# Kernel optimization log

Measured on AMD Instinct MI355X. Metric: run time of the kernel, lower is better.

The kernel has to match this reference:

```python
import jax, jax.numpy as jnp
import numpy as np
from jax import lax

B, C, L = 32, 64, 16384
C_OUT = 64


def conv1d(x, w, b):
    # x: [B,C,L], w: [Cout,Cin,K], b: [Cout]
    y = lax.conv_general_dilated(x, w, window_strides=(1,), padding='VALID',
                                 dimension_numbers=('NCH', 'OIH', 'NCH'))
    return y + b[None, :, None]


def setup_inputs() -> dict:
    key = jax.random.key(0)
    k1, k2, k3, k4, k5 = jax.random.split(key, 5)
    x = jax.random.normal(k1, (B, C, L), dtype=jnp.float32)
    # kernel_size = 1 (see shape_source); PyTorch Conv1d default init scale ~ 1/sqrt(Cin*K)
    s = 1.0 / np.sqrt(C * 1)
    offset_w = jax.random.uniform(k2, (C * 1, C, 1), jnp.float32, -s, s)
    offset_b = jax.random.uniform(k3, (C * 1,), jnp.float32, -s, s)
    regular_w = jax.random.uniform(k4, (C_OUT, C, 1), jnp.float32, -s, s)
    regular_b = jax.random.uniform(k5, (C_OUT,), jnp.float32, -s, s)
    return {'x': x, 'offset_w': offset_w, 'offset_b': offset_b,
            'regular_w': regular_w, 'regular_b': regular_b}


def reference(x, offset_w, offset_b, regular_w, regular_b):
    Bx, Cx, Lx = x.shape
    offsets = conv1d(x, offset_w, offset_b)                 # [B,C,L]
    base = jnp.arange(Lx, dtype=x.dtype)[None, None, :]      # [1,1,L]
    indices = jnp.clip(base + offsets, 0.0, Lx - 1)          # [B,C,L] float positions
    idx_floor = jnp.floor(indices)
    idx_ceil = jnp.ceil(indices)
    x_floor = jnp.take_along_axis(x, idx_floor.astype(jnp.int32), axis=2)
    x_ceil = jnp.take_along_axis(x, idx_ceil.astype(jnp.int32), axis=2)
    frac = indices - idx_floor
    x_deform = (1.0 - frac) * x_floor + frac * x_ceil        # [B,C,L]
    return conv1d(x_deform, regular_w, regular_b)            # [B,Cout,L]
```

## Files before the change

kernel.cpp:

```cpp
#include <hip/hip_runtime.h>


#define BDIM 256
#define BB   32
#define CC   64
#define LL   16384
#define TL   64
#define HH   4
#define ROWS (TL + 2*HH)
#define RSW  36
#define RSH  72

typedef __fp16 half_t;
typedef __attribute__((ext_vector_type(2))) __fp16 h2;
typedef __attribute__((ext_vector_type(8))) __fp16 h8;
typedef __attribute__((ext_vector_type(4))) float f4;

union H2U { h2 h; unsigned u; };
union H8U { unsigned u[4]; h8 v; };

static __device__ __forceinline__ unsigned pk(float a, float b) {
    H2U r; r.h = __builtin_amdgcn_cvt_pkrtz(a, b); return r.u;
}

static __device__ __forceinline__ void load_a_split(const float* __restrict__ wp,
                                                    int row, int ks, int q,
                                                    h8* ahi, h8* alo) {
    const float* base = wp + row * 64 + ks * 32 + q * 8;
    float4 w0 = *(const float4*)base;
    float4 w1 = *(const float4*)(base + 4);
    float v[8] = {w0.x, w0.y, w0.z, w0.w, w1.x, w1.y, w1.z, w1.w};
    H8U h, l;
    #pragma unroll
    for (int p = 0; p < 4; ++p) {
        H2U hh; hh.h = __builtin_amdgcn_cvt_pkrtz(v[2*p], v[2*p+1]);
        h.u[p] = hh.u;
        l.u[p] = pk(v[2*p] - (float)hh.h[0], v[2*p+1] - (float)hh.h[1]);
    }
    *ahi = h.v; *alo = l.v;
}

static __device__ __forceinline__ h8 load_a_f16(const float* __restrict__ wp,
                                                int row, int ks, int q) {
    const float* base = wp + row * 64 + ks * 32 + q * 8;
    float4 w0 = *(const float4*)base;
    float4 w1 = *(const float4*)(base + 4);
    float v[8] = {w0.x, w0.y, w0.z, w0.w, w1.x, w1.y, w1.z, w1.w};
    H8U r;
    #pragma unroll
    for (int p = 0; p < 4; ++p) r.u[p] = pk(v[2*p], v[2*p+1]);
    return r.v;
}

__global__ __launch_bounds__(BDIM)
void deform_conv1d_r5(const float* __restrict__ x,
                      const float* __restrict__ offw,
                      const float* __restrict__ offb,
                      const float* __restrict__ regw,
                      const float* __restrict__ regb,
                      float* __restrict__ out) {
    __shared__ __align__(16) unsigned char smem[10368 + 9216];
    unsigned* XtH = (unsigned*)smem;
    unsigned* XdW = (unsigned*)(smem + 10368);
    half_t*   XtHh = (half_t*)smem;
    half_t*   Xdh  = (half_t*)(smem + 10368);
    (void)Xdh;

    const int tid = threadIdx.x;
    const int bx  = blockIdx.x;
    const int lg0 = bx * TL;
    const int b   = blockIdx.y;
    const size_t xb = (size_t)b * CC * LL;

    if (bx >= 1 && bx <= (LL / TL) - 2) {
        for (int i = tid; i < 288; i += BDIM) {
            int cb = i / 18, lb = i - cb * 18;
            int c0 = cb * 4;
            int l0 = lg0 - HH + lb * 4;
            const float* pp = x + xb + (size_t)c0 * LL + l0;
            float4 v0 = *(const float4*)(pp);
            float4 v1 = *(const float4*)(pp + LL);
            float4 v2 = *(const float4*)(pp + 2 * LL);
            float4 v3 = *(const float4*)(pp + 3 * LL);
            float e0[4] = {v0.x, v0.y, v0.z, v0.w};
            float e1[4] = {v1.x, v1.y, v1.z, v1.w};
            float e2[4] = {v2.x, v2.y, v2.z, v2.w};
            float e3[4] = {v3.x, v3.y, v3.z, v3.w};
            int blkw  = (cb >> 1) ^ (lb & 7);
            int wbase = (4 * lb) * RSW + (blkw << 2) + 2 * (cb & 1);
            #pragma unroll
            for (int rl = 0; rl < 4; ++rl) {
                uint2 hw;
                hw.x = pk(e0[rl], e1[rl]);
                hw.y = pk(e2[rl], e3[rl]);
                *(uint2*)&XtH[wbase + rl * RSW] = hw;
            }
        }
    } else {
        for (int i = tid; i < ROWS * CC; i += BDIM) {
            int r = i >> 6, c = i & 63;
            int g = min(max(lg0 - HH + r, 0), LL - 1);
            float v = x[xb + (size_t)c * LL + g];
            int blk = (c >> 3) ^ ((r >> 2) & 7);
            XtHh[r * RSH + (blk << 3) + (c & 7)] = (half_t)v;
        }
    }

    const int wv   = tid >> 6;
    const int lane = tid & 63;
    const int q    = lane >> 4;
    const int n    = lane & 15;

    h8 ahi[2], alo[2];
    load_a_split(offw, 16 * wv + n, 0, q, &ahi[0], &alo[0]);
    load_a_split(offw, 16 * wv + n, 1, q, &ahi[1], &alo[1]);
    f4 acc[4];
    {
        float4 bo = *(const float4*)(offb + 16 * wv + 4 * q);
        #pragma unroll
        for (int nt = 0; nt < 4; ++nt) acc[nt] = (f4){bo.x, bo.y, bo.z, bo.w};
    }
    __syncthreads();

    #pragma unroll
    for (int nt = 0; nt < 4; ++nt) {
        const int r  = 16 * nt + n + HH;
        const int rb = r * RSW;
        const int sb = (r >> 2) & 7;
        #pragma unroll
        for (int ks = 0; ks < 2; ++ks) {
            int blk = (4 * ks + q) ^ sb;
            h8 bv = *(const h8*)&XtH[rb + (blk << 2)];
            acc[nt] = __builtin_amdgcn_mfma_f32_16x16x32_f16(ahi[ks], bv, acc[nt], 0, 0, 0);
            acc[nt] = __builtin_amdgcn_mfma_f32_16x16x32_f16(alo[ks], bv, acc[nt], 0, 0, 0);
        }
    }

    #pragma unroll
    for (int nt = 0; nt < 4; ++nt) {
        const int l = lg0 + 16 * nt + n;
        #pragma unroll
        for (int reg = 0; reg < 4; ++reg) {
            const int c = 16 * wv + 4 * q + reg;
            float o  = acc[nt][reg];
            float p  = (float)l + o;
            p = __builtin_amdgcn_fmed3f(p, 0.0f, (float)(LL - 1));
            float of = floorf(p);
            float fr = p - of;
            int idx  = (int)of;
            int u    = idx - lg0 + HH;
            float x0, x1;
            if ((unsigned)u <= (unsigned)(ROWS - 2)) {
                int b0 = (c >> 3) ^ ((u >> 2) & 7);
                int b1 = (c >> 3) ^ (((u + 1) >> 2) & 7);
                x0 = (float)XtHh[u * RSH + (b0 << 3) + (c & 7)];
                x1 = (float)XtHh[(u + 1) * RSH + (b1 << 3) + (c & 7)];
            } else {
                const float* xr = x + xb + (size_t)c * LL;
                x0 = xr[idx];
                x1 = xr[idx + (fr > 0.0f ? 1 : 0)];
            }
            acc[nt][reg] = x0 + fr * (x1 - x0);
        }
    }

    #pragma unroll
    for (int nt = 0; nt < 4; ++nt) {
        const int row = 16 * nt + n;
        const int sb  = (row >> 2) & 7;
        const int bw  = (2 * wv + (q >> 1)) ^ sb;
        uint2 pw;
        pw.x = pk(acc[nt][0], acc[nt][1]);
        pw.y = pk(acc[nt][2], acc[nt][3]);
        *(uint2*)&XdW[row * RSW + (bw << 2) + 2 * (q & 1)] = pw;
    }

    h8 a2[2];
    a2[0] = load_a_f16(regw, 16 * wv + n, 0, q);
    a2[1] = load_a_f16(regw, 16 * wv + n, 1, q);
    {
        float4 br = *(const float4*)(regb + 16 * wv + 4 * q);
        #pragma unroll
        for (int nt = 0; nt < 4; ++nt) acc[nt] = (f4){br.x, br.y, br.z, br.w};
    }
    __syncthreads();

    #pragma unroll
    for (int nt = 0; nt < 4; ++nt) {
        const int row = 16 * nt + n;
        const int sb  = (row >> 2) & 7;
        #pragma unroll
        for (int ks = 0; ks < 2; ++ks) {
            int blk = (4 * ks + q) ^ sb;
            h8 bv = *(const h8*)&XdW[row * RSW + (blk << 2)];
            acc[nt] = __builtin_amdgcn_mfma_f32_16x16x32_f16(a2[ks], bv, acc[nt], 0, 0, 0);
        }
    }

    float* op = out + (size_t)b * CC * LL;
    #pragma unroll
    for (int nt = 0; nt < 4; ++nt) {
        #pragma unroll
        for (int reg = 0; reg < 4; ++reg) {
            op[(size_t)(16 * wv + 4 * q + reg) * LL + lg0 + 16 * nt + n] = acc[nt][reg];
        }
    }
}

extern "C" void kernel_launch(void* const* d_in, const int* in_sizes, int n_in,
                              void* d_out, int out_size, void* d_ws, size_t ws_size,
                              hipStream_t stream) {
    const float* x    = (const float*)d_in[0];
    const float* offw = (const float*)d_in[1];
    const float* offb = (const float*)d_in[2];
    const float* regw = (const float*)d_in[3];
    const float* regb = (const float*)d_in[4];
    float* out = (float*)d_out;

    dim3 grid(LL / TL, BB);
    deform_conv1d_r5<<<grid, dim3(BDIM), 0, stream>>>(x, offw, offb, regw, regb, out);
}
```

Baseline: 256.8 us.

## Process four tiles per block with double-buffered staging and halo reuse

```diff
diff --git a/kernel.cpp b/kernel.cpp
--- a/kernel.cpp
+++ b/kernel.cpp
@@ -10,6 +10,8 @@
 #define ROWS (TL + 2*HH)
 #define RSW  36
 #define RSH  72
+#define NT   4
+#define XTB  10368
 
 typedef __fp16 half_t;
 typedef __attribute__((ext_vector_type(2))) __fp16 h2;
@@ -52,158 +54,203 @@
     return r.v;
 }
 
+static __device__ __forceinline__ void stage_write4(unsigned* dst, int cb, int rowb,
+                                                    const float4& v0, const float4& v1,
+                                                    const float4& v2, const float4& v3) {
+    float a0[4] = {v0.x, v0.y, v0.z, v0.w};
+    float a1[4] = {v1.x, v1.y, v1.z, v1.w};
+    float a2[4] = {v2.x, v2.y, v2.z, v2.w};
+    float a3[4] = {v3.x, v3.y, v3.z, v3.w};
+    int wbase = rowb * RSW + (((cb >> 1) ^ ((rowb >> 2) & 7)) << 2) + 2 * (cb & 1);
+    #pragma unroll
+    for (int rl = 0; rl < 4; ++rl) {
+        uint2 hw;
+        hw.x = pk(a0[rl], a1[rl]);
+        hw.y = pk(a2[rl], a3[rl]);
+        *(uint2*)&dst[wbase + rl * RSW] = hw;
+    }
+}
+
 __global__ __launch_bounds__(BDIM)
-void deform_conv1d_r5(const float* __restrict__ x,
+void deform_conv1d_r6(const float* __restrict__ x,
                       const float* __restrict__ offw,
                       const float* __restrict__ offb,
                       const float* __restrict__ regw,
                       const float* __restrict__ regb,
                       float* __restrict__ out) {
-    __shared__ __align__(16) unsigned char smem[10368 + 9216];
-    unsigned* XtH = (unsigned*)smem;
-    unsigned* XdW = (unsigned*)(smem + 10368);
-    half_t*   XtHh = (half_t*)smem;
-    half_t*   Xdh  = (half_t*)(smem + 10368);
-    (void)Xdh;
+    __shared__ __align__(16) unsigned char smem[2 * XTB + 9216];
+    unsigned* XdW = (unsigned*)(smem + 2 * XTB);
 
     const int tid = threadIdx.x;
     const int bx  = blockIdx.x;
-    const int lg0 = bx * TL;
     const int b   = blockIdx.y;
     const size_t xb = (size_t)b * CC * LL;
-
-    if (bx >= 1 && bx <= (LL / TL) - 2) {
-        for (int i = tid; i < 288; i += BDIM) {
-            int cb = i / 18, lb = i - cb * 18;
-            int c0 = cb * 4;
-            int l0 = lg0 - HH + lb * 4;
-            const float* pp = x + xb + (size_t)c0 * LL + l0;
-            float4 v0 = *(const float4*)(pp);
-            float4 v1 = *(const float4*)(pp + LL);
-            float4 v2 = *(const float4*)(pp + 2 * LL);
-            float4 v3 = *(const float4*)(pp + 3 * LL);
-            float e0[4] = {v0.x, v0.y, v0.z, v0.w};
-            float e1[4] = {v1.x, v1.y, v1.z, v1.w};
-            float e2[4] = {v2.x, v2.y, v2.z, v2.w};
-            float e3[4] = {v3.x, v3.y, v3.z, v3.w};
-            int blkw  = (cb >> 1) ^ (lb & 7);
-            int wbase = (4 * lb) * RSW + (blkw << 2) + 2 * (cb & 1);
-            #pragma unroll
-            for (int rl = 0; rl < 4; ++rl) {
-                uint2 hw;
-                hw.x = pk(e0[rl], e1[rl]);
-                hw.y = pk(e2[rl], e3[rl]);
-                *(uint2*)&XtH[wbase + rl * RSW] = hw;
-            }
-        }
-    } else {
-        for (int i = tid; i < ROWS * CC; i += BDIM) {
-            int r = i >> 6, c = i & 63;
-            int g = min(max(lg0 - HH + r, 0), LL - 1);
-            float v = x[xb + (size_t)c * LL + g];
-            int blk = (c >> 3) ^ ((r >> 2) & 7);
-            XtHh[r * RSH + (blk << 3) + (c & 7)] = (half_t)v;
-        }
-    }
 
     const int wv   = tid >> 6;
     const int lane = tid & 63;
     const int q    = lane >> 4;
     const int n    = lane & 15;
-
-    h8 ahi[2], alo[2];
+    const int scb  = tid >> 4;
+    const int slb  = tid & 15;
+
+    {
+        const int lg0 = (NT * bx) * TL;
+        unsigned* dst = (unsigned*)smem;
+        half_t*  dsth = (half_t*)smem;
+        if (bx == 0) {
+            for (int i = tid; i < ROWS * CC; i += BDIM) {
+                int r = i >> 6, c = i & 63;
+                int g = min(max(lg0 - HH + r, 0), LL - 1);
+                float v = x[xb + (size_t)c * LL + g];
+                int blk = (c >> 3) ^ ((r >> 2) & 7);
+                dsth[r * RSH + (blk << 3) + (c & 7)] = (half_t)v;
+            }
+        } else {
+            const float* pp = x + xb + (size_t)(4 * scb) * LL + (lg0 + 4 + 4 * slb);
+            float4 v0 = *(const float4*)pp;
+            float4 v1 = *(const float4*)(pp + LL);
+            float4 v2 = *(const float4*)(pp + 2 * LL);
+            float4 v3 = *(const float4*)(pp + 3 * LL);
+            stage_write4(dst, scb, 8 + 4 * slb, v0, v1, v2, v3);
+            if (tid < 32) {
+                int lb2 = tid & 1, cb2 = tid >> 1;
+                const float* p2 = x + xb + (size_t)(4 * cb2) * LL + (lg0 - 4 + 4 * lb2);
+                float4 u0 = *(const float4*)p2;
+                float4 u1 = *(const float4*)(p2 + LL);
+                float4 u2 = *(const float4*)(p2 + 2 * LL);
+                float4 u3 = *(const float4*)(p2 + 3 * LL);
+                stage_write4(dst, cb2, 4 * lb2, u0, u1, u2, u3);
+            }
+        }
+    }
+
+    h8 ahi[2], alo[2], a2f[2];
     load_a_split(offw, 16 * wv + n, 0, q, &ahi[0], &alo[0]);
     load_a_split(offw, 16 * wv + n, 1, q, &ahi[1], &alo[1]);
-    f4 acc[4];
-    {
-        float4 bo = *(const float4*)(offb + 16 * wv + 4 * q);
+    a2f[0] = load_a_f16(regw, 16 * wv + n, 0, q);
+    a2f[1] = load_a_f16(regw, 16 * wv + n, 1, q);
+    float4 bo = *(const float4*)(offb + 16 * wv + 4 * q);
+    float4 br = *(const float4*)(regb + 16 * wv + 4 * q);
+    __syncthreads();
+
+    #pragma unroll
+    for (int tt = 0; tt < NT; ++tt) {
+        const int lg0 = (NT * bx + tt) * TL;
+        unsigned* Xc  = (unsigned*)(smem + (tt & 1) * XTB);
+        unsigned* Xn  = (unsigned*)(smem + ((tt & 1) ^ 1) * XTB);
+        half_t*   Xch = (half_t*)Xc;
+        const bool has_next  = (tt < NT - 1);
+        const bool next_fast = has_next && !(bx == 63 && tt == NT - 2);
+
+        float4 s0, s1, s2, s3;
+        if (next_fast) {
+            const float* pp = x + xb + (size_t)(4 * scb) * LL + (lg0 + TL + 4 + 4 * slb);
+            s0 = *(const float4*)pp;
+            s1 = *(const float4*)(pp + LL);
+            s2 = *(const float4*)(pp + 2 * LL);
+            s3 = *(const float4*)(pp + 3 * LL);
+        }
+
+        f4 acc[4];
         #pragma unroll
         for (int nt = 0; nt < 4; ++nt) acc[nt] = (f4){bo.x, bo.y, bo.z, bo.w};
-    }
-    __syncthreads();
-
-    #pragma unroll
-    for (int nt = 0; nt < 4; ++nt) {
-        const int r  = 16 * nt + n + HH;
-        const int rb = r * RSW;
-        const int sb = (r >> 2) & 7;
-        #pragma unroll
-        for (int ks = 0; ks < 2; ++ks) {
-            int blk = (4 * ks + q) ^ sb;
-            h8 bv = *(const h8*)&XtH[rb + (blk << 2)];
-            acc[nt] = __builtin_amdgcn_mfma_f32_16x16x32_f16(ahi[ks], bv, acc[nt], 0, 0, 0);
-            acc[nt] = __builtin_amdgcn_mfma_f32_16x16x32_f16(alo[ks], bv, acc[nt], 0, 0, 0);
-        }
-    }
-
-    #pragma unroll
-    for (int nt = 0; nt < 4; ++nt) {
-        const int l = lg0 + 16 * nt + n;
-        #pragma unroll
-        for (int reg = 0; reg < 4; ++reg) {
-            const int c = 16 * wv + 4 * q + reg;
-            float o  = acc[nt][reg];
-            float p  = (float)l + o;
-            p = __builtin_amdgcn_fmed3f(p, 0.0f, (float)(LL - 1));
-            float of = floorf(p);
-            float fr = p - of;
-            int idx  = (int)of;
-            int u    = idx - lg0 + HH;
-            float x0, x1;
-            if ((unsigned)u <= (unsigned)(ROWS - 2)) {
-                int b0 = (c >> 3) ^ ((u >> 2) & 7);
-                int b1 = (c >> 3) ^ (((u + 1) >> 2) & 7);
-                x0 = (float)XtHh[u * RSH + (b0 << 3) + (c & 7)];
-                x1 = (float)XtHh[(u + 1) * RSH + (b1 << 3) + (c & 7)];
+        #pragma unroll
+        for (int nt = 0; nt < 4; ++nt) {
+            const int r  = 16 * nt + n + HH;
+            const int rb = r * RSW;
+            const int sb = (r >> 2) & 7;
+            #pragma unroll
+            for (int ks = 0; ks < 2; ++ks) {
+                int blk = (4 * ks + q) ^ sb;
+                h8 bv = *(const h8*)&Xc[rb + (blk << 2)];
+                acc[nt] = __builtin_amdgcn_mfma_f32_16x16x32_f16(ahi[ks], bv, acc[nt], 0, 0, 0);
+                acc[nt] = __builtin_amdgcn_mfma_f32_16x16x32_f16(alo[ks], bv, acc[nt], 0, 0, 0);
+            }
+        }
+
+        #pragma unroll
+        for (int nt = 0; nt < 4; ++nt) {
+            const int l = lg0 + 16 * nt + n;
+            #pragma unroll
+            for (int reg = 0; reg < 4; ++reg) {
+                const int c = 16 * wv + 4 * q + reg;
+                float o  = acc[nt][reg];
+                float p  = (float)l + o;
+                p = __builtin_amdgcn_fmed3f(p, 0.0f, (float)(LL - 1));
+                float of = floorf(p);
+                float fr = p - of;
+                int idx  = (int)of;
+                int u    = idx - lg0 + HH;
+                float x0, x1;
+                if ((unsigned)u <= (unsigned)(ROWS - 2)) {
+                    int b0 = (c >> 3) ^ ((u >> 2) & 7);
+                    int b1 = (c >> 3) ^ (((u + 1) >> 2) & 7);
+                    x0 = (float)Xch[u * RSH + (b0 << 3) + (c & 7)];
+                    x1 = (float)Xch[(u + 1) * RSH + (b1 << 3) + (c & 7)];
+                } else {
+                    const float* xr = x + xb + (size_t)c * LL;
+                    x0 = xr[idx];
+                    x1 = xr[idx + (fr > 0.0f ? 1 : 0)];
+                }
+                acc[nt][reg] = x0 + fr * (x1 - x0);
+            }
+        }
+
+        #pragma unroll
+        for (int nt = 0; nt < 4; ++nt) {
+            const int row = 16 * nt + n;
+            const int sb  = (row >> 2) & 7;
+            const int bw  = (2 * wv + (q >> 1)) ^ sb;
+            uint2 pw;
+            pw.x = pk(acc[nt][0], acc[nt][1]);
+            pw.y = pk(acc[nt][2], acc[nt][3]);
+            *(uint2*)&XdW[row * RSW + (bw << 2) + 2 * (q & 1)] = pw;
+        }
+
+        if (has_next) {
+            if (tid < 144) {
+                int j  = tid / 18;
+                int k2 = (tid - 18 * j) * 2;
+                *(uint2*)&Xn[j * RSW + k2] = *(const uint2*)&Xc[(64 + j) * RSW + k2];
+            }
+            if (next_fast) {
+                stage_write4(Xn, scb, 8 + 4 * slb, s0, s1, s2, s3);
             } else {
-                const float* xr = x + xb + (size_t)c * LL;
-                x0 = xr[idx];
-                x1 = xr[idx + (fr > 0.0f ? 1 : 0)];
-            }
-            acc[nt][reg] = x0 + fr * (x1 - x0);
-        }
-    }
-
-    #pragma unroll
-    for (int nt = 0; nt < 4; ++nt) {
-        const int row = 16 * nt + n;
-        const int sb  = (row >> 2) & 7;
-        const int bw  = (2 * wv + (q >> 1)) ^ sb;
-        uint2 pw;
-        pw.x = pk(acc[nt][0], acc[nt][1]);
-        pw.y = pk(acc[nt][2], acc[nt][3]);
-        *(uint2*)&XdW[row * RSW + (bw << 2) + 2 * (q & 1)] = pw;
-    }
-
-    h8 a2[2];
-    a2[0] = load_a_f16(regw, 16 * wv + n, 0, q);
-    a2[1] = load_a_f16(regw, 16 * wv + n, 1, q);
-    {
-        float4 br = *(const float4*)(regb + 16 * wv + 4 * q);
+                half_t* Xnh = (half_t*)Xn;
+                for (int i = tid; i < TL * CC; i += BDIM) {
+                    int r = 8 + (i >> 6), c = i & 63;
+                    int g = min(lg0 + TL - HH + r, LL - 1);
+                    float v = x[xb + (size_t)c * LL + g];
+                    int blk = (c >> 3) ^ ((r >> 2) & 7);
+                    Xnh[r * RSH + (blk << 3) + (c & 7)] = (half_t)v;
+                }
+            }
+        }
+        __syncthreads();
+
         #pragma unroll
         for (int nt = 0; nt < 4; ++nt) acc[nt] = (f4){br.x, br.y, br.z, br.w};
-    }
-    __syncthreads();
-
-    #pragma unroll
-    for (int nt = 0; nt < 4; ++nt) {
-        const int row = 16 * nt + n;
-        const int sb  = (row >> 2) & 7;
-        #pragma unroll
-        for (int ks = 0; ks < 2; ++ks) {
-            int blk = (4 * ks + q) ^ sb;
-            h8 bv = *(const h8*)&XdW[row * RSW + (blk << 2)];
-            acc[nt] = __builtin_amdgcn_mfma_f32_16x16x32_f16(a2[ks], bv, acc[nt], 0, 0, 0);
-        }
-    }
-
-    float* op = out + (size_t)b * CC * LL;
-    #pragma unroll
-    for (int nt = 0; nt < 4; ++nt) {
-        #pragma unroll
-        for (int reg = 0; reg < 4; ++reg) {
-            op[(size_t)(16 * wv + 4 * q + reg) * LL + lg0 + 16 * nt + n] = acc[nt][reg];
-        }
+        #pragma unroll
+        for (int nt = 0; nt < 4; ++nt) {
+            const int row = 16 * nt + n;
+            const int sb  = (row >> 2) & 7;
+            #pragma unroll
+            for (int ks = 0; ks < 2; ++ks) {
+                int blk = (4 * ks + q) ^ sb;
+                h8 bv = *(const h8*)&XdW[row * RSW + (blk << 2)];
+                acc[nt] = __builtin_amdgcn_mfma_f32_16x16x32_f16(a2f[ks], bv, acc[nt], 0, 0, 0);
+            }
+        }
+
+        float* op = out + (size_t)b * CC * LL;
+        #pragma unroll
+        for (int nt = 0; nt < 4; ++nt) {
+            #pragma unroll
+            for (int reg = 0; reg < 4; ++reg) {
+                op[(size_t)(16 * wv + 4 * q + reg) * LL + lg0 + 16 * nt + n] = acc[nt][reg];
+            }
+        }
+        if (tt < NT - 1) __syncthreads();
     }
 }
 
@@ -217,6 +264,6 @@
     const float* regb = (const float*)d_in[4];
     float* out = (float*)d_out;
 
-    dim3 grid(LL / TL, BB);
-    deform_conv1d_r5<<<grid, dim3(BDIM), 0, stream>>>(x, offw, offb, regw, regb, out);
-}
+    dim3 grid(LL / TL / NT, BB);
+    deform_conv1d_r6<<<grid, dim3(BDIM), 0, stream>>>(x, offw, offb, regw, regb, out);
+}
```

Result: no change. 258.1 us (+0.5%).
